# Kernel optimization log

Hardware: AMD Instinct MI355X
Metric: run time of the kernel (lower is better)

The kernel has to match this reference:

```python
import jax, jax.numpy as jnp
import numpy as np

B, T, V, E, H, O = 32, 512, 32000, 512, 1024, 128


def setup_inputs() -> dict:
    key = jax.random.key(0)
    ks = jax.random.split(key, 8)
    s = lambda k, shape: (jax.random.normal(k, shape) * 0.02).astype(jnp.float32)
    return {
        "tokens": jax.random.randint(ks[0], (B, T), 0, V),
        "verb_indices": jax.random.randint(ks[1], (B,), 0, T),
        "emb": s(ks[2], (V, E)),
        "W_ih": s(ks[3], (4 * H, E)),
        "W_hh": s(ks[4], (4 * H, H)),
        "b_ih": jnp.zeros((4 * H,), jnp.float32),
        "b_hh": jnp.zeros((4 * H,), jnp.float32),
        "W_lin": s(ks[5], (O, 2 * H)),
        "b_lin": jnp.zeros((O,), jnp.float32),
    }


def _lstm(e, W_ih, W_hh, b_ih, b_hh):
    # e: [B,T,E] -> hidden states [B,T,H]; PyTorch gate order i,f,g,o
    Hd = W_hh.shape[1]
    # precompute input projections for all timesteps (one big GEMM)
    x_proj = jnp.einsum("bte,ge->btg", e, W_ih) + b_ih + b_hh  # [B,T,4H]

    def step(carry, x_t):
        h, c = carry
        gates = x_t + h @ W_hh.T  # [B,4H]
        i, f, g, o = jnp.split(gates, 4, axis=-1)
        i = jax.nn.sigmoid(i)
        f = jax.nn.sigmoid(f)
        g = jnp.tanh(g)
        o = jax.nn.sigmoid(o)
        c = f * c + i * g
        h = o * jnp.tanh(c)
        return (h, c), h

    h0 = jnp.zeros((e.shape[0], Hd), e.dtype)
    (_, _), hs = jax.lax.scan(step, (h0, h0), jnp.swapaxes(x_proj, 0, 1))
    return jnp.swapaxes(hs, 0, 1)  # [B,T,H]


def reference(tokens, verb_indices, emb, W_ih, W_hh, b_ih, b_hh, W_lin, b_lin):
    e = emb[tokens]  # [B,T,E]
    out = _lstm(e, W_ih, W_hh, b_ih, b_hh)  # [B,T,H]
    verbs = out[jnp.arange(out.shape[0]), verb_indices]  # [B,H] verb hidden state
    # linear over concat([verb, out_t]) == split the weight and sum two GEMMs
    Wv, Wo = jnp.split(W_lin, 2, axis=1)  # [O,H] each
    logits = (
        jnp.einsum("bh,oh->bo", verbs, Wv)[:, None, :]
        + jnp.einsum("bth,oh->bto", out, Wo)
        + b_lin
    )  # [B,T,O]
    return jax.nn.log_softmax(logits, axis=-1)
```

## Files before the change

kernel.cpp:

```cpp
#include <hip/hip_runtime.h>


typedef short s8v __attribute__((ext_vector_type(8)));
typedef float f4v __attribute__((ext_vector_type(4)));
typedef unsigned int u4v __attribute__((ext_vector_type(4)));

#define WS_CNT_OFF   131072
#define WS_VROWS_OFF 139264
#define WS_VLOG_OFF  204800

__device__ __forceinline__ float b2f(unsigned short u) {
    union { unsigned int i; float f; } x; x.i = ((unsigned int)u) << 16; return x.f;
}
__device__ __forceinline__ unsigned short f2b(float f) {
    union { float f; unsigned int i; } x; x.f = f;
    unsigned int r = (x.i + 0x7fffu + ((x.i >> 16) & 1u)) >> 16;
    return (unsigned short)r;
}
__device__ __forceinline__ float blo(unsigned int u) {
    union { unsigned int i; float f; } x; x.i = u << 16; return x.f;
}
__device__ __forceinline__ float bhi(unsigned int u) {
    union { unsigned int i; float f; } x; x.i = u & 0xffff0000u; return x.f;
}

__global__ void init_kernel(unsigned int* ws) {
    int i = blockIdx.x * 256 + threadIdx.x;
    if (i < 34816) ws[i] = 0u;
}

__device__ __forceinline__ void project_cols(
    const short* hA, const float* __restrict__ Wr0, const float* __restrict__ Wr1,
    float* __restrict__ dout, int b0, int tproj, int w, int tid)
{
    const int pair = tid >> 4, p = tid & 15;
    const int b = pair >> 1, oc = pair & 1;
    const float* wr = oc ? Wr1 : Wr0;
    float acc = 0.f;
#pragma unroll
    for (int j = 0; j < 8; ++j) {
        int ko = j * 16 + p;
        u4v d = *(const u4v*)&hA[(ko * 17 + b) * 8];
        const float* wk = wr + ko * 8;
        f4v w0 = *(const f4v*)wk, w1 = *(const f4v*)(wk + 4);
        unsigned int d0 = d[0], d1 = d[1], d2 = d[2], d3 = d[3];
        acc += blo(d0) * w0[0] + bhi(d0) * w0[1] + blo(d1) * w0[2] + bhi(d1) * w0[3]
             + blo(d2) * w1[0] + bhi(d2) * w1[1] + blo(d3) * w1[2] + bhi(d3) * w1[3];
    }
#pragma unroll
    for (int off = 1; off < 16; off <<= 1) acc += __shfl_xor(acc, off);
    if (p == 0)
        dout[((size_t)(b0 + b) * 512 + tproj) * 128 + 2 * w + oc] = acc;
}

__global__ __launch_bounds__(256, 1) void scan_kernel(
    const int* __restrict__ tokens,
    const int* __restrict__ vidx,
    const float* __restrict__ emb,
    const float* __restrict__ W_ih,
    const float* __restrict__ W_hh,
    const float* __restrict__ b_ih,
    const float* __restrict__ b_hh,
    const float* __restrict__ W_lin,
    unsigned short* __restrict__ hbuf,
    unsigned int* __restrict__ flags_all,
    unsigned short* __restrict__ vrows,
    float* __restrict__ dout)
{
    __shared__ short hA[128 * 17 * 8];
    __shared__ short eA[2][64 * 17 * 8];
    __shared__ int   tokL[512 * 8];

    const int tid  = threadIdx.x;
    const int g    = blockIdx.x >> 6;
    const int w    = blockIdx.x & 63;
    const int b0   = g * 8;
    const int lane = tid & 63;
    const int v    = tid >> 6;
    const int q    = lane >> 4;
    const int c    = lane & 15;

    const float* Wr0 = W_lin + (size_t)(2 * w) * 2048 + 1024;
    const float* Wr1 = W_lin + (size_t)(2 * w + 1) * 2048 + 1024;

    const int n = ((c >> 2) * 1024) + 16 * w + 4 * v + (c & 3);
    s8v Bh[32], Be[16];
    {
        const float* rh = W_hh + (size_t)n * 1024;
#pragma unroll
        for (int ks = 0; ks < 32; ++ks) {
            const float* s = rh + ks * 32 + q * 8;
            f4v lo = *(const f4v*)s, hi = *(const f4v*)(s + 4);
            s8v f;
#pragma unroll
            for (int j = 0; j < 4; ++j) { f[j] = (short)f2b(lo[j]); f[j + 4] = (short)f2b(hi[j]); }
            Bh[ks] = f;
        }
        const float* re = W_ih + (size_t)n * 512;
#pragma unroll
        for (int ks = 0; ks < 16; ++ks) {
            const float* s = re + ks * 32 + q * 8;
            f4v lo = *(const f4v*)s, hi = *(const f4v*)(s + 4);
            s8v f;
#pragma unroll
            for (int j = 0; j < 4; ++j) { f[j] = (short)f2b(lo[j]); f[j + 4] = (short)f2b(hi[j]); }
            Be[ks] = f;
        }
    }

    for (int i = tid; i < 4096; i += 256)
        tokL[(i & 511) * 8 + (i >> 9)] = tokens[(b0 + (i >> 9)) * 512 + (i & 511)];

    const s8v zv = {0,0,0,0,0,0,0,0};
    for (int i = tid; i < 1024; i += 256) { int ko = i >> 3, r = 8 + (i & 7);
        *(s8v*)&hA[(ko * 17 + r) * 8] = zv; }
    for (int i = tid; i < 512; i += 256) { int ko = i >> 3, r = 8 + (i & 7);
        *(s8v*)&eA[0][(ko * 17 + r) * 8] = zv;
        *(s8v*)&eA[1][(ko * 17 + r) * 8] = zv; }
    __syncthreads();

    for (int i = tid; i < 512; i += 256) {
        int ko = i >> 3, b = i & 7;
        int tok = tokL[b];
        const float* s = emb + (size_t)tok * 512 + ko * 8;
        f4v lo = *(const f4v*)s, hi = *(const f4v*)(s + 4);
        s8v f;
#pragma unroll
        for (int j = 0; j < 4; ++j) { f[j] = (short)f2b(lo[j]); f[j + 4] = (short)f2b(hi[j]); }
        *(s8v*)&eA[0][(ko * 17 + b) * 8] = f;
    }

    const int jloc = 16 * w + 4 * v + (lane & 3);
    const float bI = b_ih[jloc]        + b_hh[jloc];
    const float bF = b_ih[1024 + jloc] + b_hh[1024 + jloc];
    const float bG = b_ih[2048 + jloc] + b_hh[2048 + jloc];
    const float bO = b_ih[3072 + jloc] + b_hh[3072 + jloc];
    const int  shbase = (lane & 48) | (lane & 3);
    const bool stActV = ((lane & 13) == 0) && (lane < 32);
    const bool stActQ = ((lane & 15) == 0) && (lane < 32);
    const int  Dq = ((2 * w + (v >> 1)) * 32 + 2 * (v & 1) + 16 * q) >> 1;
    int tv0 = -1, tv1 = -1, tv2 = -1, tv3 = -1;
    if (stActV) {
        int bb = b0 + 4 * (lane >> 4);
        tv0 = vidx[bb]; tv1 = vidx[bb + 1]; tv2 = vidx[bb + 2]; tv3 = vidx[bb + 3];
    }
    const int vrb = (b0 + 4 * (lane >> 4)) * 1024 + jloc;

    float cst[4] = {0.f, 0.f, 0.f, 0.f};
    unsigned short*     hb     = hbuf + g * 2 * 8192;
    unsigned long long* hb64   = (unsigned long long*)hb;
    unsigned int*       gflags = flags_all + g * 2048;
    const int fidx = (lane * 4 + v) * 8;
    const int myflag = (w * 4 + v) * 8;
    int rp = 0;
    __syncthreads();

    for (int t = 0; t < 512; ++t) {
        if (t > 0) {
            const unsigned tt = (unsigned)t;
            for (int spin = 0; ; ++spin) {
                unsigned f = __hip_atomic_load(&gflags[fidx], __ATOMIC_RELAXED,
                                               __HIP_MEMORY_SCOPE_AGENT);
                if (__all(f >= tt)) break;
                if (spin >= 2) __builtin_amdgcn_s_sleep(2);
            }
            asm volatile("" ::: "memory");
        }

        const unsigned long long* src =
            (const unsigned long long*)(hb + rp * 8192);
        const short* eAc = eA[t & 1];
        f4v ae = {0.f, 0.f, 0.f, 0.f};
        {
            unsigned long long dbuf[4]; int jarr[4];
#pragma unroll
            for (int it = 0; it < 4; ++it) {
                int i = ((it + w) & 7) * 64 + lane;
                int j = (((((i >> 3) << 1) | (v >> 1)) << 4) | ((i & 7) << 1) | (v & 1));
                jarr[it] = j;
                dbuf[it] = __hip_atomic_load(src + j, __ATOMIC_RELAXED,
                                             __HIP_MEMORY_SCOPE_AGENT);
            }
#pragma unroll
            for (int ks = 0; ks < 8; ++ks) {
                s8v a = *(const s8v*)&eAc[((ks * 4 + q) * 17 + c) * 8];
                ae = __builtin_amdgcn_mfma_f32_16x16x32_bf16(a, Be[ks], ae, 0, 0, 0);
            }
#pragma unroll
            for (int it = 0; it < 4; ++it) {
                int j = jarr[it];
                int ko = j >> 4, b = (j >> 1) & 7, posq = (j & 1) << 2;
                *(unsigned long long*)&hA[(ko * 17 + b) * 8 + posq] = dbuf[it];
            }
#pragma unroll
            for (int it = 4; it < 8; ++it) {
                int i = ((it + w) & 7) * 64 + lane;
                int j = (((((i >> 3) << 1) | (v >> 1)) << 4) | ((i & 7) << 1) | (v & 1));
                jarr[it - 4] = j;
                dbuf[it - 4] = __hip_atomic_load(src + j, __ATOMIC_RELAXED,
                                                 __HIP_MEMORY_SCOPE_AGENT);
            }
#pragma unroll
            for (int ks = 8; ks < 16; ++ks) {
                s8v a = *(const s8v*)&eAc[((ks * 4 + q) * 17 + c) * 8];
                ae = __builtin_amdgcn_mfma_f32_16x16x32_bf16(a, Be[ks], ae, 0, 0, 0);
            }
#pragma unroll
            for (int it = 0; it < 4; ++it) {
                int j = jarr[it];
                int ko = j >> 4, b = (j >> 1) & 7, posq = (j & 1) << 2;
                *(unsigned long long*)&hA[(ko * 17 + b) * 8 + posq] = dbuf[it];
            }
        }
        __syncthreads();

        f4v ah0 = {0.f, 0.f, 0.f, 0.f}, ah1 = {0.f, 0.f, 0.f, 0.f};
#pragma unroll
        for (int ks = 0; ks < 16; ++ks) {
            s8v a0 = *(const s8v*)&hA[((2 * ks) * 4 + q) * 17 * 8 + c * 8];
            s8v a1 = *(const s8v*)&hA[((2 * ks + 1) * 4 + q) * 17 * 8 + c * 8];
            ah0 = __builtin_amdgcn_mfma_f32_16x16x32_bf16(a0, Bh[2 * ks], ah0, 0, 0, 0);
            ah1 = __builtin_amdgcn_mfma_f32_16x16x32_bf16(a1, Bh[2 * ks + 1], ah1, 0, 0, 0);
        }

        int hui[4];
#pragma unroll
        for (int r = 0; r < 4; ++r) {
            float s = ae[r] + ah0[r] + ah1[r];
            float xi = __shfl(s, shbase);
            float xf = __shfl(s, shbase + 4);
            float xg = __shfl(s, shbase + 8);
            float xo = __shfl(s, shbase + 12);
            float ig = 1.f / (1.f + __expf(-(xi + bI)));
            float fg = 1.f / (1.f + __expf(-(xf + bF)));
            float gg = 1.f - 2.f / (1.f + __expf(2.f * (xg + bG)));
            float og = 1.f / (1.f + __expf(-(xo + bO)));
            cst[r] = fg * cst[r] + ig * gg;
            float h = og * (1.f - 2.f / (1.f + __expf(2.f * cst[r])));
            hui[r] = (int)f2b(h);
        }
#pragma unroll
        for (int r = 0; r < 4; ++r) {
            int ph = __shfl_xor(hui[r], 1);
            unsigned pack = (unsigned)hui[r] | (((unsigned)ph) << 16);
            unsigned hi = (unsigned)__shfl_xor((int)pack, 2);
            if (stActQ) {
                unsigned long long pk = (unsigned long long)pack |
                                        (((unsigned long long)hi) << 32);
                __hip_atomic_store(&hb64[(rp ^ 1) * 1024 + Dq + r * 2], pk,
                                   __ATOMIC_RELAXED, __HIP_MEMORY_SCOPE_AGENT);
            }
            if (stActV) {
                int tvr = (r == 0) ? tv0 : (r == 1) ? tv1 : (r == 2) ? tv2 : tv3;
                if (t == tvr)
                    *(unsigned int*)&vrows[vrb + r * 1024] = pack;
            }
        }
        asm volatile("s_waitcnt vmcnt(0)" ::: "memory");
        if (lane == 0)
            __hip_atomic_store(&gflags[myflag], (unsigned)(t + 1),
                               __ATOMIC_RELAXED, __HIP_MEMORY_SCOPE_AGENT);

        if (t >= 1)
            project_cols(hA, Wr0, Wr1, dout, b0, t - 1, w, tid);

        if (t < 511) {
            int tn = t + 1;
            short* eAn = eA[tn & 1];
            for (int i = tid; i < 512; i += 256) {
                int ko = i >> 3, b = i & 7;
                int tok = tokL[tn * 8 + b];
                const float* s2 = emb + (size_t)tok * 512 + ko * 8;
                f4v lo = *(const f4v*)s2, hi = *(const f4v*)(s2 + 4);
                s8v f;
#pragma unroll
                for (int j2 = 0; j2 < 4; ++j2) { f[j2] = (short)f2b(lo[j2]); f[j2 + 4] = (short)f2b(hi[j2]); }
                *(s8v*)&eAn[(ko * 17 + b) * 8] = f;
            }
        }
        __syncthreads();
        rp ^= 1;
    }

    for (int spin = 0; ; ++spin) {
        unsigned f = __hip_atomic_load(&gflags[fidx], __ATOMIC_RELAXED,
                                       __HIP_MEMORY_SCOPE_AGENT);
        if (__all(f >= 512u)) break;
        if (spin >= 2) __builtin_amdgcn_s_sleep(2);
    }
    asm volatile("" ::: "memory");
    {
        const unsigned long long* src = (const unsigned long long*)(hb + rp * 8192);
#pragma unroll
        for (int it = 0; it < 8; ++it) {
            int i = ((it + w) & 7) * 64 + lane;
            int j = (((((i >> 3) << 1) | (v >> 1)) << 4) | ((i & 7) << 1) | (v & 1));
            unsigned long long d = __hip_atomic_load(src + j, __ATOMIC_RELAXED,
                                                     __HIP_MEMORY_SCOPE_AGENT);
            int ko = j >> 4, b = (j >> 1) & 7, posq = (j & 1) << 2;
            *(unsigned long long*)&hA[(ko * 17 + b) * 8 + posq] = d;
        }
    }
    __syncthreads();
    project_cols(hA, Wr0, Wr1, dout, b0, 511, w, tid);
}

__global__ void verb_kernel(const unsigned short* __restrict__ vrows,
                            const float* __restrict__ W_lin,
                            const float* __restrict__ b_lin,
                            float* __restrict__ vlog)
{
    __shared__ float vrow[1024];
    int b = blockIdx.x, tid = threadIdx.x;
    for (int i = tid; i < 1024; i += 256) vrow[i] = b2f(vrows[b * 1024 + i]);
    __syncthreads();
    if (tid < 128) {
        float acc = 0.f;
        const float* wr = W_lin + (size_t)tid * 2048;
        for (int h = 0; h < 1024; ++h) acc += vrow[h] * wr[h];
        vlog[b * 128 + tid] = acc + b_lin[tid];
    }
}

__global__ void softmax_kernel(float* __restrict__ dout,
                               const float* __restrict__ vlog)
{
    int tid = threadIdx.x;
    int grow = blockIdx.x * 32 + (tid >> 3);
    int part = tid & 7;
    int b = grow >> 9;
    float* pp = dout + (size_t)grow * 128 + part * 16;
    const float* vb = vlog + b * 128 + part * 16;
    float L[16];
#pragma unroll
    for (int i = 0; i < 16; ++i) L[i] = pp[i] + vb[i];
    float m = L[0];
#pragma unroll
    for (int i = 1; i < 16; ++i) m = fmaxf(m, L[i]);
    for (int off = 1; off < 8; off <<= 1) m = fmaxf(m, __shfl_xor(m, off));
    float s = 0.f;
#pragma unroll
    for (int i = 0; i < 16; ++i) s += expf(L[i] - m);
    for (int off = 1; off < 8; off <<= 1) s += __shfl_xor(s, off);
    float lz = m + logf(s);
#pragma unroll
    for (int i = 0; i < 16; ++i) pp[i] = L[i] - lz;
}

extern "C" void kernel_launch(void* const* d_in, const int* in_sizes, int n_in,
                              void* d_out, int out_size, void* d_ws, size_t ws_size,
                              hipStream_t stream) {
    const int*   tokens = (const int*)d_in[0];
    const int*   vidx   = (const int*)d_in[1];
    const float* emb    = (const float*)d_in[2];
    const float* W_ih   = (const float*)d_in[3];
    const float* W_hh   = (const float*)d_in[4];
    const float* b_ih   = (const float*)d_in[5];
    const float* b_hh   = (const float*)d_in[6];
    const float* W_lin  = (const float*)d_in[7];
    const float* b_lin  = (const float*)d_in[8];
    float* dout = (float*)d_out;

    char* ws = (char*)d_ws;
    unsigned short* hbuf  = (unsigned short*)ws;
    unsigned int*   flags = (unsigned int*)(ws + WS_CNT_OFF);
    unsigned short* vrows = (unsigned short*)(ws + WS_VROWS_OFF);
    float*          vlog  = (float*)(ws + WS_VLOG_OFF);

    init_kernel<<<136, 256, 0, stream>>>((unsigned int*)ws);
    scan_kernel<<<256, 256, 0, stream>>>(tokens, vidx, emb, W_ih, W_hh, b_ih, b_hh,
                                         W_lin, hbuf, flags, vrows, dout);
    verb_kernel<<<32, 256, 0, stream>>>(vrows, W_lin, b_lin, vlog);
    softmax_kernel<<<512, 256, 0, stream>>>(dout, vlog);
}
```

Before: 3.321 ms.

## Replace flag-based step barrier with self-validating encoded h buffers, fuse verb projection

Drops the per-step flag counters and spin-wait. Each h value is XOR-encoded so it can never be zero, which lets readers poll the data words directly. A triple-buffered ring is used, and each step re-zeroes the buffer that will be written two steps later. The separate verb_kernel is removed: the verb-row logits are computed inside the scan from the shared h tile, and b_lin is now added in softmax. The aim is to shorten the cross-block synchronization latency on every timestep. The cost is per-word polling loops, extra zeroing stores, and reliance on the encoding never producing zero.

```diff
diff --git a/kernel.cpp b/kernel.cpp
--- a/kernel.cpp
+++ b/kernel.cpp
@@ -5,9 +5,8 @@
 typedef float f4v __attribute__((ext_vector_type(4)));
 typedef unsigned int u4v __attribute__((ext_vector_type(4)));
 
-#define WS_CNT_OFF   131072
-#define WS_VROWS_OFF 139264
-#define WS_VLOG_OFF  204800
+#define WS_VLOG_OFF 196608
+#define ENC_MASK 0x7F807F807F807F80ULL
 
 __device__ __forceinline__ float b2f(unsigned short u) {
     union { unsigned int i; float f; } x; x.i = ((unsigned int)u) << 16; return x.f;
@@ -26,7 +25,7 @@
 
 __global__ void init_kernel(unsigned int* ws) {
     int i = blockIdx.x * 256 + threadIdx.x;
-    if (i < 34816) ws[i] = 0u;
+    if (i < 53248) ws[i] = 0u;
 }
 
 __device__ __forceinline__ void project_cols(
@@ -51,6 +50,30 @@
     for (int off = 1; off < 16; off <<= 1) acc += __shfl_xor(acc, off);
     if (p == 0)
         dout[((size_t)(b0 + b) * 512 + tproj) * 128 + 2 * w + oc] = acc;
+}
+
+__device__ __forceinline__ void verb_cols(
+    const short* hA, const float* __restrict__ W_lin, float* __restrict__ vlog,
+    int b0, int w, int tid, const int* tvL, int tprev)
+{
+    const int pair = tid >> 4, p = tid & 15;
+    const int bb = pair >> 1, oc = pair & 1;
+    if (tvL[bb] != tprev) return;
+    const float* wr = W_lin + (size_t)(2 * w + oc) * 2048;
+    float acc = 0.f;
+#pragma unroll
+    for (int j = 0; j < 8; ++j) {
+        int ko = j * 16 + p;
+        u4v d = *(const u4v*)&hA[(ko * 17 + bb) * 8];
+        const float* wk = wr + ko * 8;
+        f4v w0 = *(const f4v*)wk, w1 = *(const f4v*)(wk + 4);
+        acc += blo(d[0]) * w0[0] + bhi(d[0]) * w0[1] + blo(d[1]) * w0[2] + bhi(d[1]) * w0[3]
+             + blo(d[2]) * w1[0] + bhi(d[2]) * w1[1] + blo(d[3]) * w1[2] + bhi(d[3]) * w1[3];
+    }
+#pragma unroll
+    for (int off = 1; off < 16; off <<= 1) acc += __shfl_xor(acc, off);
+    if (p == 0)
+        vlog[(b0 + bb) * 128 + 2 * w + oc] = acc;
 }
 
 __global__ __launch_bounds__(256, 1) void scan_kernel(
@@ -63,13 +86,13 @@
     const float* __restrict__ b_hh,
     const float* __restrict__ W_lin,
     unsigned short* __restrict__ hbuf,
-    unsigned int* __restrict__ flags_all,
-    unsigned short* __restrict__ vrows,
+    float* __restrict__ vlog,
     float* __restrict__ dout)
 {
     __shared__ short hA[128 * 17 * 8];
     __shared__ short eA[2][64 * 17 * 8];
     __shared__ int   tokL[512 * 8];
+    __shared__ int   tvL[8];
 
     const int tid  = threadIdx.x;
     const int g    = blockIdx.x >> 6;
@@ -110,9 +133,10 @@
 
     for (int i = tid; i < 4096; i += 256)
         tokL[(i & 511) * 8 + (i >> 9)] = tokens[(b0 + (i >> 9)) * 512 + (i & 511)];
+    if (tid < 8) tvL[tid] = vidx[b0 + tid];
 
     const s8v zv = {0,0,0,0,0,0,0,0};
-    for (int i = tid; i < 1024; i += 256) { int ko = i >> 3, r = 8 + (i & 7);
+    for (int i = tid; i < 2048; i += 256) { int ko = i >> 4, r = i & 15;
         *(s8v*)&hA[(ko * 17 + r) * 8] = zv; }
     for (int i = tid; i < 512; i += 256) { int ko = i >> 3, r = 8 + (i & 7);
         *(s8v*)&eA[0][(ko * 17 + r) * 8] = zv;
@@ -136,83 +160,73 @@
     const float bG = b_ih[2048 + jloc] + b_hh[2048 + jloc];
     const float bO = b_ih[3072 + jloc] + b_hh[3072 + jloc];
     const int  shbase = (lane & 48) | (lane & 3);
-    const bool stActV = ((lane & 13) == 0) && (lane < 32);
     const bool stActQ = ((lane & 15) == 0) && (lane < 32);
-    const int  Dq = ((2 * w + (v >> 1)) * 32 + 2 * (v & 1) + 16 * q) >> 1;
-    int tv0 = -1, tv1 = -1, tv2 = -1, tv3 = -1;
-    if (stActV) {
-        int bb = b0 + 4 * (lane >> 4);
-        tv0 = vidx[bb]; tv1 = vidx[bb + 1]; tv2 = vidx[bb + 2]; tv3 = vidx[bb + 3];
-    }
-    const int vrb = (b0 + 4 * (lane >> 4)) * 1024 + jloc;
+    const int  Dq = (2 * w + (v >> 1)) * 16 + (v & 1) + 8 * q;
 
     float cst[4] = {0.f, 0.f, 0.f, 0.f};
-    unsigned short*     hb     = hbuf + g * 2 * 8192;
-    unsigned long long* hb64   = (unsigned long long*)hb;
-    unsigned int*       gflags = flags_all + g * 2048;
-    const int fidx = (lane * 4 + v) * 8;
-    const int myflag = (w * 4 + v) * 8;
-    int rp = 0;
+    unsigned long long* hb64 = (unsigned long long*)(hbuf + g * 3 * 8192);
+    int rd = 2, wr = 0, zr = 1;
     __syncthreads();
 
     for (int t = 0; t < 512; ++t) {
-        if (t > 0) {
-            const unsigned tt = (unsigned)t;
-            for (int spin = 0; ; ++spin) {
-                unsigned f = __hip_atomic_load(&gflags[fidx], __ATOMIC_RELAXED,
-                                               __HIP_MEMORY_SCOPE_AGENT);
-                if (__all(f >= tt)) break;
-                if (spin >= 2) __builtin_amdgcn_s_sleep(2);
-            }
-            asm volatile("" ::: "memory");
-        }
-
-        const unsigned long long* src =
-            (const unsigned long long*)(hb + rp * 8192);
+        const unsigned long long* src = hb64 + rd * 2048;
         const short* eAc = eA[t & 1];
         f4v ae = {0.f, 0.f, 0.f, 0.f};
-        {
-            unsigned long long dbuf[4]; int jarr[4];
-#pragma unroll
-            for (int it = 0; it < 4; ++it) {
-                int i = ((it + w) & 7) * 64 + lane;
-                int j = (((((i >> 3) << 1) | (v >> 1)) << 4) | ((i & 7) << 1) | (v & 1));
-                jarr[it] = j;
-                dbuf[it] = __hip_atomic_load(src + j, __ATOMIC_RELAXED,
-                                             __HIP_MEMORY_SCOPE_AGENT);
-            }
-#pragma unroll
-            for (int ks = 0; ks < 8; ++ks) {
+        if (t > 0) {
+            unsigned long long d[8];
+#pragma unroll
+            for (int it = 0; it < 8; ++it) {
+                int j = ((it + w) & 7) * 256 + tid;
+                d[it] = __hip_atomic_load(src + j, __ATOMIC_RELAXED,
+                                          __HIP_MEMORY_SCOPE_AGENT);
+            }
+            asm volatile("" ::: "memory");
+#pragma unroll
+            for (int ks = 0; ks < 16; ++ks) {
                 s8v a = *(const s8v*)&eAc[((ks * 4 + q) * 17 + c) * 8];
                 ae = __builtin_amdgcn_mfma_f32_16x16x32_bf16(a, Be[ks], ae, 0, 0, 0);
             }
-#pragma unroll
-            for (int it = 0; it < 4; ++it) {
-                int j = jarr[it];
-                int ko = j >> 4, b = (j >> 1) & 7, posq = (j & 1) << 2;
-                *(unsigned long long*)&hA[(ko * 17 + b) * 8 + posq] = dbuf[it];
-            }
-#pragma unroll
-            for (int it = 4; it < 8; ++it) {
-                int i = ((it + w) & 7) * 64 + lane;
-                int j = (((((i >> 3) << 1) | (v >> 1)) << 4) | ((i & 7) << 1) | (v & 1));
-                jarr[it - 4] = j;
-                dbuf[it - 4] = __hip_atomic_load(src + j, __ATOMIC_RELAXED,
-                                                 __HIP_MEMORY_SCOPE_AGENT);
-            }
-#pragma unroll
-            for (int ks = 8; ks < 16; ++ks) {
+            unsigned pend = 255u;
+            while (pend) {
+                unsigned np = 0;
+#pragma unroll
+                for (int it = 0; it < 8; ++it) {
+                    if (pend & (1u << it)) {
+                        if (d[it] != 0ULL) {
+                            unsigned long long dd = d[it] ^ ENC_MASK;
+                            int j = ((it + w) & 7) * 256 + tid;
+                            int ko = j >> 4, b = (j >> 1) & 7, posq = (j & 1) << 2;
+                            *(unsigned long long*)&hA[(ko * 17 + b) * 8 + posq] = dd;
+                        } else {
+                            np |= 1u << it;
+                        }
+                    }
+                }
+#pragma unroll
+                for (int it = 0; it < 8; ++it) {
+                    if (np & (1u << it)) {
+                        int j = ((it + w) & 7) * 256 + tid;
+                        d[it] = __hip_atomic_load(src + j, __ATOMIC_RELAXED,
+                                                  __HIP_MEMORY_SCOPE_AGENT);
+                    }
+                }
+                pend = np;
+            }
+        } else {
+#pragma unroll
+            for (int ks = 0; ks < 16; ++ks) {
                 s8v a = *(const s8v*)&eAc[((ks * 4 + q) * 17 + c) * 8];
                 ae = __builtin_amdgcn_mfma_f32_16x16x32_bf16(a, Be[ks], ae, 0, 0, 0);
             }
-#pragma unroll
-            for (int it = 0; it < 4; ++it) {
-                int j = jarr[it];
-                int ko = j >> 4, b = (j >> 1) & 7, posq = (j & 1) << 2;
-                *(unsigned long long*)&hA[(ko * 17 + b) * 8 + posq] = dbuf[it];
-            }
         }
         __syncthreads();
+
+        if (stActQ) {
+#pragma unroll
+            for (int r = 0; r < 4; ++r)
+                __hip_atomic_store(&hb64[zr * 2048 + Dq + r * 2], 0ULL,
+                                   __ATOMIC_RELAXED, __HIP_MEMORY_SCOPE_AGENT);
+        }
 
         f4v ah0 = {0.f, 0.f, 0.f, 0.f}, ah1 = {0.f, 0.f, 0.f, 0.f};
 #pragma unroll
@@ -239,30 +253,24 @@
             float h = og * (1.f - 2.f / (1.f + __expf(2.f * cst[r])));
             hui[r] = (int)f2b(h);
         }
+        asm volatile("s_waitcnt vmcnt(0)" ::: "memory");
 #pragma unroll
         for (int r = 0; r < 4; ++r) {
-            int ph = __shfl_xor(hui[r], 1);
-            unsigned pack = (unsigned)hui[r] | (((unsigned)ph) << 16);
+            int phh = __shfl_xor(hui[r], 1);
+            unsigned pack = (unsigned)hui[r] | (((unsigned)phh) << 16);
             unsigned hi = (unsigned)__shfl_xor((int)pack, 2);
             if (stActQ) {
-                unsigned long long pk = (unsigned long long)pack |
-                                        (((unsigned long long)hi) << 32);
-                __hip_atomic_store(&hb64[(rp ^ 1) * 1024 + Dq + r * 2], pk,
+                unsigned long long pk = ((unsigned long long)pack |
+                                         (((unsigned long long)hi) << 32)) ^ ENC_MASK;
+                __hip_atomic_store(&hb64[wr * 2048 + Dq + r * 2], pk,
                                    __ATOMIC_RELAXED, __HIP_MEMORY_SCOPE_AGENT);
             }
-            if (stActV) {
-                int tvr = (r == 0) ? tv0 : (r == 1) ? tv1 : (r == 2) ? tv2 : tv3;
-                if (t == tvr)
-                    *(unsigned int*)&vrows[vrb + r * 1024] = pack;
-            }
-        }
-        asm volatile("s_waitcnt vmcnt(0)" ::: "memory");
-        if (lane == 0)
-            __hip_atomic_store(&gflags[myflag], (unsigned)(t + 1),
-                               __ATOMIC_RELAXED, __HIP_MEMORY_SCOPE_AGENT);
-
-        if (t >= 1)
+        }
+
+        if (t >= 1) {
             project_cols(hA, Wr0, Wr1, dout, b0, t - 1, w, tid);
+            verb_cols(hA, W_lin, vlog, b0, w, tid, tvL, t - 1);
+        }
 
         if (t < 511) {
             int tn = t + 1;
@@ -279,51 +287,53 @@
             }
         }
         __syncthreads();
-        rp ^= 1;
-    }
-
-    for (int spin = 0; ; ++spin) {
-        unsigned f = __hip_atomic_load(&gflags[fidx], __ATOMIC_RELAXED,
-                                       __HIP_MEMORY_SCOPE_AGENT);
-        if (__all(f >= 512u)) break;
-        if (spin >= 2) __builtin_amdgcn_s_sleep(2);
-    }
-    asm volatile("" ::: "memory");
+        int nrd = wr; wr = zr; zr = rd; rd = nrd;
+    }
+
     {
-        const unsigned long long* src = (const unsigned long long*)(hb + rp * 8192);
+        const unsigned long long* src = hb64 + rd * 2048;
+        unsigned long long d[8];
 #pragma unroll
         for (int it = 0; it < 8; ++it) {
-            int i = ((it + w) & 7) * 64 + lane;
-            int j = (((((i >> 3) << 1) | (v >> 1)) << 4) | ((i & 7) << 1) | (v & 1));
-            unsigned long long d = __hip_atomic_load(src + j, __ATOMIC_RELAXED,
-                                                     __HIP_MEMORY_SCOPE_AGENT);
-            int ko = j >> 4, b = (j >> 1) & 7, posq = (j & 1) << 2;
-            *(unsigned long long*)&hA[(ko * 17 + b) * 8 + posq] = d;
+            int j = ((it + w) & 7) * 256 + tid;
+            d[it] = __hip_atomic_load(src + j, __ATOMIC_RELAXED,
+                                      __HIP_MEMORY_SCOPE_AGENT);
+        }
+        unsigned pend = 255u;
+        while (pend) {
+            unsigned np = 0;
+#pragma unroll
+            for (int it = 0; it < 8; ++it) {
+                if (pend & (1u << it)) {
+                    if (d[it] != 0ULL) {
+                        unsigned long long dd = d[it] ^ ENC_MASK;
+                        int j = ((it + w) & 7) * 256 + tid;
+                        int ko = j >> 4, b = (j >> 1) & 7, posq = (j & 1) << 2;
+                        *(unsigned long long*)&hA[(ko * 17 + b) * 8 + posq] = dd;
+                    } else {
+                        np |= 1u << it;
+                    }
+                }
+            }
+#pragma unroll
+            for (int it = 0; it < 8; ++it) {
+                if (np & (1u << it)) {
+                    int j = ((it + w) & 7) * 256 + tid;
+                    d[it] = __hip_atomic_load(src + j, __ATOMIC_RELAXED,
+                                              __HIP_MEMORY_SCOPE_AGENT);
+                }
+            }
+            pend = np;
         }
     }
     __syncthreads();
     project_cols(hA, Wr0, Wr1, dout, b0, 511, w, tid);
-}
-
-__global__ void verb_kernel(const unsigned short* __restrict__ vrows,
-                            const float* __restrict__ W_lin,
-                            const float* __restrict__ b_lin,
-                            float* __restrict__ vlog)
-{
-    __shared__ float vrow[1024];
-    int b = blockIdx.x, tid = threadIdx.x;
-    for (int i = tid; i < 1024; i += 256) vrow[i] = b2f(vrows[b * 1024 + i]);
-    __syncthreads();
-    if (tid < 128) {
-        float acc = 0.f;
-        const float* wr = W_lin + (size_t)tid * 2048;
-        for (int h = 0; h < 1024; ++h) acc += vrow[h] * wr[h];
-        vlog[b * 128 + tid] = acc + b_lin[tid];
-    }
+    verb_cols(hA, W_lin, vlog, b0, w, tid, tvL, 511);
 }
 
 __global__ void softmax_kernel(float* __restrict__ dout,
-                               const float* __restrict__ vlog)
+                               const float* __restrict__ vlog,
+                               const float* __restrict__ b_lin)
 {
     int tid = threadIdx.x;
     int grow = blockIdx.x * 32 + (tid >> 3);
@@ -331,9 +341,10 @@
     int b = grow >> 9;
     float* pp = dout + (size_t)grow * 128 + part * 16;
     const float* vb = vlog + b * 128 + part * 16;
+    const float* bl = b_lin + part * 16;
     float L[16];
 #pragma unroll
-    for (int i = 0; i < 16; ++i) L[i] = pp[i] + vb[i];
+    for (int i = 0; i < 16; ++i) L[i] = pp[i] + vb[i] + bl[i];
     float m = L[0];
 #pragma unroll
     for (int i = 1; i < 16; ++i) m = fmaxf(m, L[i]);
@@ -362,14 +373,11 @@
     float* dout = (float*)d_out;
 
     char* ws = (char*)d_ws;
-    unsigned short* hbuf  = (unsigned short*)ws;
-    unsigned int*   flags = (unsigned int*)(ws + WS_CNT_OFF);
-    unsigned short* vrows = (unsigned short*)(ws + WS_VROWS_OFF);
-    float*          vlog  = (float*)(ws + WS_VLOG_OFF);
-
-    init_kernel<<<136, 256, 0, stream>>>((unsigned int*)ws);
+    unsigned short* hbuf = (unsigned short*)ws;
+    float*          vlog = (float*)(ws + WS_VLOG_OFF);
+
+    init_kernel<<<208, 256, 0, stream>>>((unsigned int*)ws);
     scan_kernel<<<256, 256, 0, stream>>>(tokens, vidx, emb, W_ih, W_hh, b_ih, b_hh,
-                                         W_lin, hbuf, flags, vrows, dout);
-    verb_kernel<<<32, 256, 0, stream>>>(vrows, W_lin, b_lin, vlog);
-    softmax_kernel<<<512, 256, 0, stream>>>(dout, vlog);
-}
+                                         W_lin, hbuf, vlog, dout);
+    softmax_kernel<<<512, 256, 0, stream>>>(dout, vlog, b_lin);
+}
```

Result: no change. 3.297 ms (-0.7%).
